# Performance work log

Hardware: AMD Instinct MI355X
Metric: run time of the kernel (lower is better)

The kernel has to match this reference:

```python
import jax, jax.numpy as jnp
import numpy as np
import math

D = 768
H = 12
DFF = 3072
HD = D // H


def _layernorm(x, g, b, eps=1e-5):
    mu = jnp.mean(x, axis=-1, keepdims=True)
    var = jnp.var(x, axis=-1, keepdims=True)
    return (x - mu) * jax.lax.rsqrt(var + eps) * g + b


def setup_inputs() -> dict:
    key = jax.random.key(0)
    ks = jax.random.split(key, 12)
    B, S = 2, 4096
    s = 1.0 / math.sqrt(D)
    sf = 1.0 / math.sqrt(DFF)
    return {
        "x": jax.random.normal(ks[0], (B, S, D), jnp.float32),
        "attention_mask": jnp.ones((B, S), jnp.int32),
        "ln1_g": jnp.ones((D,), jnp.float32),
        "ln1_b": jnp.zeros((D,), jnp.float32),
        "ln2_g": jnp.ones((D,), jnp.float32),
        "ln2_b": jnp.zeros((D,), jnp.float32),
        "Wq": jax.random.normal(ks[1], (D, D), jnp.float32) * s,
        "bq": jnp.zeros((D,), jnp.float32),
        "Wk": jax.random.normal(ks[2], (D, D), jnp.float32) * s,
        "bk": jnp.zeros((D,), jnp.float32),
        "Wv": jax.random.normal(ks[3], (D, D), jnp.float32) * s,
        "bv": jnp.zeros((D,), jnp.float32),
        "Wo": jax.random.normal(ks[4], (D, D), jnp.float32) * s,
        "bo": jnp.zeros((D,), jnp.float32),
        "W1": jax.random.normal(ks[5], (D, DFF), jnp.float32) * s,
        "b1": jnp.zeros((DFF,), jnp.float32),
        "W2": jax.random.normal(ks[6], (DFF, D), jnp.float32) * sf,
        "b2": jnp.zeros((D,), jnp.float32),
    }


def _block(x, attention_mask, ln1_g, ln1_b, ln2_g, ln2_b,
           Wq, bq, Wk, bk, Wv, bv, Wo, bo, W1, b1, W2, b2):
    B, S, _ = x.shape
    h = _layernorm(x, ln1_g, ln1_b)
    q = (h @ Wq + bq).reshape(B, S, H, HD)
    k = (h @ Wk + bk).reshape(B, S, H, HD)
    v = (h @ Wv + bv).reshape(B, S, H, HD)
    # scores: [B, H, S, S]
    dots = jnp.einsum('bqhd,bkhd->bhqk', q, k) / math.sqrt(HD)
    causal = jnp.tril(jnp.ones((S, S), bool))  # True = keep
    keep = causal[None, None] & (attention_mask != 0)[:, None, None, :]
    dots = jnp.where(keep, dots, -jnp.inf)
    probs = jax.nn.softmax(dots, axis=-1)
    ctx = jnp.einsum('bhqk,bkhd->bqhd', probs, v).reshape(B, S, D)
    sa = ctx @ Wo + bo  # dropout = identity (eval)
    x = x + sa
    h2 = _layernorm(x, ln2_g, ln2_b)
    ff = jax.nn.relu(h2 @ W1 + b1) @ W2 + b2
    return x + ff


def reference(x, attention_mask, ln1_g, ln1_b, ln2_g, ln2_b,
              Wq, bq, Wk, bk, Wv, bv, Wo, bo, W1, b1, W2, b2):
    return _block(x, attention_mask, ln1_g, ln1_b, ln2_g, ln2_b,
                  Wq, bq, Wk, bk, Wv, bv, Wo, bo, W1, b1, W2, b2)
```

## Files before the change

### kernel.cpp

```cpp
#include <hip/hip_runtime.h>
#include <hip/hip_bf16.h>
#include <math.h>

#define S_LEN 4096
#define DMODEL 768
#define NHEAD 12
#define HDIM 64
#define DFF_ 3072
#define MROWS 8192

typedef __bf16 bf16;
typedef __bf16 bf16x4 __attribute__((ext_vector_type(4)));
typedef __bf16 bf16x8 __attribute__((ext_vector_type(8)));
typedef float f32x4 __attribute__((ext_vector_type(4)));
typedef float f32x16 __attribute__((ext_vector_type(16)));
typedef short s16x4 __attribute__((ext_vector_type(4)));
typedef s16x4 frag4;

union F4 { float4 v; float f[4]; };
union U2 { bf16 h[2]; unsigned u; };
union P4 { unsigned u[2]; frag4 v; };

__device__ __forceinline__ void gld_lds16(void* lds, const void* g) {
    __builtin_amdgcn_global_load_lds(
        (const __attribute__((address_space(1))) unsigned int*)g,
        (__attribute__((address_space(3))) unsigned int*)lds, 16, 0, 0);
}

__device__ __forceinline__ f32x4 mfma16(frag4 a, frag4 b, f32x4 c) {
#if __has_builtin(__builtin_amdgcn_mfma_f32_16x16x16bf16_1k)
    return __builtin_amdgcn_mfma_f32_16x16x16bf16_1k(a, b, c, 0, 0, 0);
#else
    union { frag4 s; bf16x4 h; } ua, ub; ua.s = a; ub.s = b;
    bf16x8 a8 = {ua.h[0], ua.h[1], ua.h[2], ua.h[3],
                 (bf16)0.f, (bf16)0.f, (bf16)0.f, (bf16)0.f};
    bf16x8 b8 = {ub.h[0], ub.h[1], ub.h[2], ub.h[3],
                 (bf16)0.f, (bf16)0.f, (bf16)0.f, (bf16)0.f};
    return __builtin_amdgcn_mfma_f32_16x16x32_bf16(a8, b8, c, 0, 0, 0);
#endif
}

__global__ __launch_bounds__(256) void pre_kernel(
    const float* __restrict__ Wq, const float* __restrict__ Wk,
    const float* __restrict__ Wv, const float* __restrict__ Wo,
    const float* __restrict__ W1, const float* __restrict__ W2,
    bf16* __restrict__ Wqt, bf16* __restrict__ Wkt, bf16* __restrict__ Wvt,
    bf16* __restrict__ Wot, bf16* __restrict__ W1t, bf16* __restrict__ W2t,
    const float* __restrict__ x, const float* __restrict__ g,
    const float* __restrict__ bta, bf16* __restrict__ hout) {
    const int tid = threadIdx.x;
    if (blockIdx.x < 1728) {
        int t = blockIdx.x;
        const float* W; bf16* Wt; int K, N;
        if      (t < 144)  { W = Wq; Wt = Wqt; K = 768;  N = 768;  }
        else if (t < 288)  { W = Wk; Wt = Wkt; K = 768;  N = 768;  t -= 144; }
        else if (t < 432)  { W = Wv; Wt = Wvt; K = 768;  N = 768;  t -= 288; }
        else if (t < 576)  { W = Wo; Wt = Wot; K = 768;  N = 768;  t -= 432; }
        else if (t < 1152) { W = W1; Wt = W1t; K = 768;  N = 3072; t -= 576; }
        else               { W = W2; Wt = W2t; K = 3072; N = 768;  t -= 1152; }
        const int nx = N >> 6;
        const int n0 = (t % nx) * 64, k0 = (t / nx) * 64;
        __shared__ float tile[64][65];
        const int lr = tid >> 4, lc = (tid & 15) << 2;
#pragma unroll
        for (int i = 0; i < 4; ++i) {
            const int r = lr + i * 16;
            F4 w; w.v = *(const float4*)&W[(size_t)(k0 + r) * N + n0 + lc];
#pragma unroll
            for (int j = 0; j < 4; ++j) tile[r][lc + j] = w.f[j];
        }
        __syncthreads();
#pragma unroll
        for (int i = 0; i < 4; ++i) {
            const int n = lr + i * 16;
            bf16x4 o;
#pragma unroll
            for (int j = 0; j < 4; ++j) o[j] = (bf16)tile[lc + j][n];
            *(bf16x4*)&Wt[(size_t)(n0 + n) * K + k0 + lc] = o;
        }
    } else {
        const int row = blockIdx.x - 1728;
        const float* xr = x + (size_t)row * DMODEL;
        float v0 = xr[tid], v1 = xr[tid + 256], v2 = xr[tid + 512];
        float s = v0 + v1 + v2;
        float ss = v0 * v0 + v1 * v1 + v2 * v2;
        for (int o = 32; o > 0; o >>= 1) {
            s += __shfl_down(s, o, 64);
            ss += __shfl_down(ss, o, 64);
        }
        __shared__ float sm[4], sm2[4];
        const int w = tid >> 6, lane = tid & 63;
        if (lane == 0) { sm[w] = s; sm2[w] = ss; }
        __syncthreads();
        s = sm[0] + sm[1] + sm[2] + sm[3];
        ss = sm2[0] + sm2[1] + sm2[2] + sm2[3];
        const float mu = s * (1.0f / DMODEL);
        const float var = ss * (1.0f / DMODEL) - mu * mu;
        const float rs = rsqrtf(var + 1e-5f);
        bf16* orow = hout + (size_t)row * DMODEL;
        orow[tid]       = (bf16)((v0 - mu) * rs * g[tid]       + bta[tid]);
        orow[tid + 256] = (bf16)((v1 - mu) * rs * g[tid + 256] + bta[tid + 256]);
        orow[tid + 512] = (bf16)((v2 - mu) * rs * g[tid + 512] + bta[tid + 512]);
    }
}

template<typename OUT>
__global__ __launch_bounds__(256) void ln_kernel(const float* __restrict__ x,
                                                 const float* __restrict__ g,
                                                 const float* __restrict__ bta,
                                                 OUT* __restrict__ out,
                                                 float* __restrict__ zb) {
    const int row = blockIdx.x;
    const int t = threadIdx.x;
    const float* xr = x + (size_t)row * DMODEL;
    float v0 = xr[t], v1 = xr[t + 256], v2 = xr[t + 512];
    float s = v0 + v1 + v2;
    float ss = v0 * v0 + v1 * v1 + v2 * v2;
    for (int o = 32; o > 0; o >>= 1) {
        s += __shfl_down(s, o, 64);
        ss += __shfl_down(ss, o, 64);
    }
    __shared__ float sm[4], sm2[4];
    const int w = t >> 6, lane = t & 63;
    if (lane == 0) { sm[w] = s; sm2[w] = ss; }
    __syncthreads();
    s = sm[0] + sm[1] + sm[2] + sm[3];
    ss = sm2[0] + sm2[1] + sm2[2] + sm2[3];
    const float mu = s * (1.0f / DMODEL);
    const float var = ss * (1.0f / DMODEL) - mu * mu;
    const float rs = rsqrtf(var + 1e-5f);
    OUT* orow = out + (size_t)row * DMODEL;
    orow[t]       = (OUT)((v0 - mu) * rs * g[t]       + bta[t]);
    orow[t + 256] = (OUT)((v1 - mu) * rs * g[t + 256] + bta[t + 256]);
    orow[t + 512] = (OUT)((v2 - mu) * rs * g[t + 512] + bta[t + 512]);
}

__global__ __launch_bounds__(256) void vtrans_kernel(const bf16* __restrict__ vb,
                                                     bf16* __restrict__ vbt) {
    const int kt = blockIdx.x, h = blockIdx.y, b = blockIdx.z;
    __shared__ bf16 tile[64][65];
    const int t = threadIdx.x;
    const int kl = t >> 2, ds = (t & 3) * 16;
    const bf16* src = vb + (size_t)(b * S_LEN + kt * 64 + kl) * DMODEL + h * HDIM + ds;
    *(bf16x8*)&tile[kl][ds]     = *(const bf16x8*)src;
    *(bf16x8*)&tile[kl][ds + 8] = *(const bf16x8*)(src + 8);
    __syncthreads();
    const int d = t >> 2;
    bf16* drow = vbt + (size_t)((b * NHEAD + h) * HDIM + d) * S_LEN + kt * 64;
#pragma unroll
    for (int c = 0; c < 2; ++c) {
        const int k0 = (t & 3) * 16 + c * 8;
        bf16x8 o;
#pragma unroll
        for (int j = 0; j < 8; ++j) o[j] = tile[k0 + j][d];
        *(bf16x8*)(drow + k0) = o;
    }
}

template<int MT, bool RELU, bool RES, bool OUT_BF16>
__global__ __launch_bounds__(256) void mgemm_kernel(
    const bf16* __restrict__ A,
    const bf16* __restrict__ Wt0, const float* __restrict__ bias0, void* __restrict__ C0,
    const bf16* __restrict__ Wt1, const float* __restrict__ bias1, void* __restrict__ C1,
    const bf16* __restrict__ Wt2, const float* __restrict__ bias2, void* __restrict__ C2,
    const float* __restrict__ R, int M, int N, int K, int Kloop,
    int koff0, int koff1, int koff2,
    float sc0, float sc1, float sc2) {
    const bf16* Wt = Wt0; const float* bias = bias0; void* C = C0; float sc = sc0; int koff = koff0;
    if (blockIdx.z == 1) { Wt = Wt1; bias = bias1; C = C1; sc = sc1; koff = koff1; }
    if (blockIdx.z == 2) { Wt = Wt2; bias = bias2; C = C2; sc = sc2; koff = koff2; }

    const int gx = gridDim.x;
    const int nwg = gx * gridDim.y;
    const int chunk = nwg >> 3;
    int lid = blockIdx.y * gx + blockIdx.x;
    lid = (lid & 7) * chunk + (lid >> 3);
    const int row0 = (lid / gx) * MT, col0 = (lid % gx) * 128;

    constexpr int NI = (MT == 128) ? 2 : 1;
    __shared__ bf16 As[2][MT * 32];
    __shared__ bf16 Bs[2][128 * 32];

    const int tid = threadIdx.x;
    const int wave = tid >> 6, lane = tid & 63;
    const int wr = (MT == 128) ? (wave >> 1) * 64 : 0;
    const int wc = (MT == 128) ? (wave & 1) * 64 : wave * 32;
    const int r5 = lane & 31, khalf = lane >> 5;
    const int rsw = (r5 >> 1) & 3;

    const int st_row = (lane >> 2);
    const int st_off = (((lane & 3) ^ ((lane >> 3) & 3)) << 4);

    f32x16 acc[2][NI] = {};

    const char* Ab = (const char*)(A + (size_t)row0 * K + koff);
    const char* Bb = (const char*)(Wt + (size_t)col0 * K + koff);
    const size_t strideA = (size_t)K * 2;

    for (int k0 = 0; k0 < Kloop; k0 += 64) {
#pragma unroll
        for (int s = 0; s < 2; ++s) {
            const int kk = k0 + s * 32;
            if (MT == 128) {
#pragma unroll
                for (int issue = 0; issue < 2; ++issue) {
                    const int r = wave * 32 + issue * 16 + st_row;
                    gld_lds16((char*)As[s] + (wave * 32 + issue * 16) * 64,
                              Ab + (size_t)r * strideA + kk * 2 + st_off);
                }
            } else {
                const int r = wave * 16 + st_row;
                gld_lds16((char*)As[s] + (wave * 16) * 64,
                          Ab + (size_t)r * strideA + kk * 2 + st_off);
            }
#pragma unroll
            for (int issue = 0; issue < 2; ++issue) {
                const int r = wave * 32 + issue * 16 + st_row;
                gld_lds16((char*)Bs[s] + (wave * 32 + issue * 16) * 64,
                          Bb + (size_t)r * strideA + kk * 2 + st_off);
            }
        }
        __syncthreads();
#pragma unroll
        for (int s = 0; s < 2; ++s) {
            bf16x8 af[2][2], bfr[NI][2];
#pragma unroll
            for (int mi = 0; mi < 2; ++mi)
#pragma unroll
                for (int kc = 0; kc < 2; ++kc)
                    af[mi][kc] = *(const bf16x8*)((const char*)As[s] +
                        (wr + mi * 32 + r5) * 64 + (((kc * 2 + khalf) ^ rsw) << 4));
#pragma unroll
            for (int ni = 0; ni < NI; ++ni)
#pragma unroll
                for (int kc = 0; kc < 2; ++kc)
                    bfr[ni][kc] = *(const bf16x8*)((const char*)Bs[s] +
                        (wc + ni * 32 + r5) * 64 + (((kc * 2 + khalf) ^ rsw) << 4));
#pragma unroll
            for (int mi = 0; mi < 2; ++mi)
#pragma unroll
                for (int ni = 0; ni < NI; ++ni)
#pragma unroll
                    for (int kc = 0; kc < 2; ++kc)
                        acc[mi][ni] = __builtin_amdgcn_mfma_f32_32x32x16_bf16(
                            bfr[ni][kc], af[mi][kc], acc[mi][ni], 0, 0, 0);
        }
        __syncthreads();
    }

#pragma unroll
    for (int ni = 0; ni < NI; ++ni) {
#pragma unroll
        for (int g = 0; g < 4; ++g) {
            const int col = col0 + wc + ni * 32 + g * 8 + khalf * 4;
            F4 bv4; bv4.v = *(const float4*)&bias[col];
#pragma unroll
            for (int mi = 0; mi < 2; ++mi) {
                const int row = row0 + wr + mi * 32 + r5;
                F4 o;
#pragma unroll
                for (int r = 0; r < 4; ++r) o.f[r] = acc[mi][ni][g * 4 + r] + bv4.f[r];
                if (RES) {
                    F4 rr; rr.v = *(const float4*)&R[(size_t)row * N + col];
#pragma unroll
                    for (int r = 0; r < 4; ++r) o.f[r] += rr.f[r];
                }
#pragma unroll
                for (int r = 0; r < 4; ++r) {
                    o.f[r] *= sc;
                    if (RELU) o.f[r] = fmaxf(o.f[r], 0.0f);
                }
                if (OUT_BF16) {
                    bf16x4 ob;
#pragma unroll
                    for (int r = 0; r < 4; ++r) ob[r] = (bf16)o.f[r];
                    *(bf16x4*)&((bf16*)C)[(size_t)row * N + col] = ob;
                } else {
                    *(float4*)&((float*)C)[(size_t)row * N + col] = o.v;
                }
            }
        }
    }
}

__global__ __launch_bounds__(256) void mattn_kernel(
    const bf16* __restrict__ Q, const bf16* __restrict__ K,
    const bf16* __restrict__ Vt, const int* __restrict__ amask,
    bf16* __restrict__ O) {
    const int bx = blockIdx.x, h = blockIdx.y, b = blockIdx.z;

    __shared__ bf16 Ks[2][4096];
    __shared__ bf16 Vs[2][4096];
    __shared__ bf16 Os[64][68];
    __shared__ float mk[2][64];
    __shared__ int flagv[2];

    const int tid = threadIdx.x;
    const int wave = tid >> 6, lane = tid & 63;
    const int l = lane & 15, quad = lane >> 4;
    const float NEG_INF = -__builtin_huge_valf();

    const int g1 = 256 + tid;
    const int rw0 = tid >> 3, pc0 = tid & 7;
    const int rw1 = g1 >> 3,  pc1 = g1 & 7;
    const int koff0 = rw0 * DMODEL + ((pc0 ^ (rw0 & 7)) << 3);
    const int koff1 = rw1 * DMODEL + ((pc1 ^ (rw1 & 7)) << 3);
    const int voff0 = rw0 * S_LEN + ((pc0 ^ (rw0 & 7)) << 3);
    const int voff1 = rw1 * S_LEN + ((pc1 ^ (rw1 & 7)) << 3);

    const bf16* Kbase = K + (size_t)b * S_LEN * DMODEL + h * HDIM;
    const bf16* Vtb = Vt + (size_t)((b * NHEAD + h) * HDIM) * S_LEN;

    const int sw = (l & 7) << 4;
    const int krd0 = l * 128 + ((quad << 4) ^ sw);
    const int krd1 = l * 128 + (((4 + quad) << 4) ^ sw);

    P4 onesu; onesu.u[0] = 0x3F803F80u; onesu.u[1] = 0x3F803F80u;
    const frag4 onesA = onesu.v;

#pragma unroll 1
    for (int pass = 0; pass < 2; ++pass) {
        const int qt = pass ? bx : (63 - bx);

        const bf16* Qb = Q + (size_t)(b * S_LEN + qt * 64 + wave * 16 + l) * DMODEL + h * HDIM;
        const bf16x8 qf0 = *(const bf16x8*)(Qb + quad * 8);
        const bf16x8 qf1 = *(const bf16x8*)(Qb + 32 + quad * 8);

        float m_run = NEG_INF;
        f32x4 acc[4] = {};
        f32x4 acc_l = {};

        {
            char* kd = (char*)Ks[0] + wave * 1024;
            char* vd = (char*)Vs[0] + wave * 1024;
            gld_lds16(kd,        Kbase + koff0);
            gld_lds16(kd + 4096, Kbase + koff1);
            gld_lds16(vd,        Vtb + voff0);
            gld_lds16(vd + 4096, Vtb + voff1);
            if (wave == 0) {
                int mv0 = amask[b * S_LEN + lane];
                mk[0][lane] = mv0 ? 0.0f : NEG_INF;
                unsigned long long bal = __ballot(mv0 != 0);
                if (lane == 0) flagv[0] = (bal == ~0ULL);
            }
        }
        __syncthreads();
        int buf = 0;
        int mv = 1;

        for (int kt = 0; kt <= qt; ++kt) {
            const bool more = (kt < qt);
            if (more) {
                const bf16* kg = Kbase + (size_t)(kt + 1) * 64 * DMODEL;
                const bf16* vg = Vtb + (kt + 1) * 64;
                const int nb = buf ^ 1;
                char* kd = (char*)Ks[nb] + wave * 1024;
                char* vd = (char*)Vs[nb] + wave * 1024;
                gld_lds16(kd,        kg + koff0);
                gld_lds16(kd + 4096, kg + koff1);
                gld_lds16(vd,        vg + voff0);
                gld_lds16(vd + 4096, vg + voff1);
                if (wave == 0) mv = amask[b * S_LEN + (kt + 1) * 64 + lane];
            }

            const int allv = flagv[buf];
            const char* Ksb = (const char*)Ks[buf];
            const char* Vsb = (const char*)Vs[buf];
            f32x4 sreg[4] = {};
            __builtin_amdgcn_s_setprio(1);
#pragma unroll
            for (int mi = 0; mi < 4; ++mi) {
                bf16x8 kf0 = *(const bf16x8*)(Ksb + mi * 2048 + krd0);
                bf16x8 kf1 = *(const bf16x8*)(Ksb + mi * 2048 + krd1);
                sreg[mi] = __builtin_amdgcn_mfma_f32_16x16x32_bf16(kf0, qf0, sreg[mi], 0, 0, 0);
                sreg[mi] = __builtin_amdgcn_mfma_f32_16x16x32_bf16(kf1, qf1, sreg[mi], 0, 0, 0);
            }
            __builtin_amdgcn_s_setprio(0);
            if (!allv) {
#pragma unroll
                for (int mi = 0; mi < 4; ++mi) {
                    F4 m4; m4.v = *(const float4*)&mk[buf][mi * 16 + quad * 4];
#pragma unroll
                    for (int r = 0; r < 4; ++r) sreg[mi][r] += m4.f[r];
                }
            }
            if (kt == qt) {
#pragma unroll
                for (int mi = 0; mi < 4; ++mi)
#pragma unroll
                    for (int r = 0; r < 4; ++r)
                        if (mi * 16 + quad * 4 + r > wave * 16 + l)
                            sreg[mi][r] = NEG_INF;
            }

            float mloc = sreg[0][0];
#pragma unroll
            for (int mi = 0; mi < 4; ++mi)
#pragma unroll
                for (int r = 0; r < 4; ++r) mloc = fmaxf(mloc, sreg[mi][r]);
            mloc = fmaxf(mloc, __shfl_xor(mloc, 16, 64));
            mloc = fmaxf(mloc, __shfl_xor(mloc, 32, 64));
            if (__any(mloc > m_run + 8.0f)) {
                const float mn = fmaxf(m_run, mloc);
                const float alpha = __builtin_amdgcn_exp2f(m_run - mn);
                m_run = mn;
#pragma unroll
                for (int di = 0; di < 4; ++di)
#pragma unroll
                    for (int r = 0; r < 4; ++r) acc[di][r] *= alpha;
#pragma unroll
                for (int r = 0; r < 4; ++r) acc_l[r] *= alpha;
            }
#pragma unroll
            for (int mi = 0; mi < 4; ++mi)
#pragma unroll
                for (int r = 0; r < 4; ++r)
                    sreg[mi][r] = __builtin_amdgcn_exp2f(sreg[mi][r] - m_run);

            unsigned pk[4][2];
#pragma unroll
            for (int mi = 0; mi < 4; ++mi) {
                U2 w0; w0.h[0] = (bf16)sreg[mi][0]; w0.h[1] = (bf16)sreg[mi][1];
                U2 w1; w1.h[0] = (bf16)sreg[mi][2]; w1.h[1] = (bf16)sreg[mi][3];
                pk[mi][0] = w0.u; pk[mi][1] = w1.u;
            }

            __builtin_amdgcn_s_setprio(1);
#pragma unroll
            for (int mi = 0; mi < 4; ++mi) {
                P4 pb; pb.u[0] = pk[mi][0]; pb.u[1] = pk[mi][1];
                const int vb_mi = (((mi << 5) | (quad << 3)) ^ sw);
#pragma unroll
                for (int di = 0; di < 4; ++di) {
                    frag4 va = *(const frag4*)(Vsb + di * 2048 + l * 128 + vb_mi);
                    acc[di] = mfma16(va, pb.v, acc[di]);
                }
                acc_l = mfma16(onesA, pb.v, acc_l);
            }
            __builtin_amdgcn_s_setprio(0);

            if (more && wave == 0) {
                const int nb = buf ^ 1;
                mk[nb][lane] = mv ? 0.0f : NEG_INF;
                unsigned long long bal = __ballot(mv != 0);
                if (lane == 0) flagv[nb] = (bal == ~0ULL);
            }
            __syncthreads();
            buf ^= 1;
        }

        const float l_fin = __shfl(acc_l[0], l, 64);
        const float rinv = 1.0f / l_fin;
#pragma unroll
        for (int mi = 0; mi < 4; ++mi) {
            U2 w0; w0.h[0] = (bf16)(acc[mi][0] * rinv); w0.h[1] = (bf16)(acc[mi][1] * rinv);
            U2 w1; w1.h[0] = (bf16)(acc[mi][2] * rinv); w1.h[1] = (bf16)(acc[mi][3] * rinv);
            *(unsigned*)&Os[wave * 16 + l][mi * 16 + quad * 4]     = w0.u;
            *(unsigned*)&Os[wave * 16 + l][mi * 16 + quad * 4 + 2] = w1.u;
        }
        __syncthreads();
        {
            const int orow = tid >> 2, oseg = (tid & 3) * 16;
            bf16* Og = O + (size_t)(b * S_LEN + qt * 64 + orow) * DMODEL + h * HDIM + oseg;
            *(bf16x8*)Og       = *(const bf16x8*)&Os[orow][oseg];
            *(bf16x8*)(Og + 8) = *(const bf16x8*)&Os[orow][oseg + 8];
        }
        __syncthreads();
    }
}

extern "C" void kernel_launch(void* const* d_in, const int* in_sizes, int n_in,
                              void* d_out, int out_size, void* d_ws, size_t ws_size,
                              hipStream_t stream) {
    const float* x     = (const float*)d_in[0];
    const int*   amask = (const int*)  d_in[1];
    const float* ln1_g = (const float*)d_in[2];
    const float* ln1_b = (const float*)d_in[3];
    const float* ln2_g = (const float*)d_in[4];
    const float* ln2_b = (const float*)d_in[5];
    const float* Wq = (const float*)d_in[6];  const float* bq = (const float*)d_in[7];
    const float* Wk = (const float*)d_in[8];  const float* bk = (const float*)d_in[9];
    const float* Wv = (const float*)d_in[10]; const float* bv = (const float*)d_in[11];
    const float* Wo = (const float*)d_in[12]; const float* bo = (const float*)d_in[13];
    const float* W1 = (const float*)d_in[14]; const float* b1 = (const float*)d_in[15];
    const float* W2 = (const float*)d_in[16]; const float* b2 = (const float*)d_in[17];
    float* out = (float*)d_out;

    char* ws = (char*)d_ws;
    const size_t WSML = (size_t)DMODEL * DMODEL * 2;
    const size_t WBIG = (size_t)DMODEL * DFF_ * 2;
    bf16* Wqt = (bf16*)(ws + 0 * WSML);
    bf16* Wkt = (bf16*)(ws + 1 * WSML);
    bf16* Wvt = (bf16*)(ws + 2 * WSML);
    bf16* Wot = (bf16*)(ws + 3 * WSML);
    bf16* W1t = (bf16*)(ws + 4 * WSML);
    bf16* W2t = (bf16*)(ws + 4 * WSML + WBIG);
    char* act = ws + 4 * WSML + 2 * WBIG;

    const size_t HB = (size_t)MROWS * DMODEL * 2;
    const size_t FB = (size_t)MROWS * DMODEL * 4;
    bf16*  h    = (bf16*)(act);
    bf16*  qb   = (bf16*)(act + HB);
    bf16*  kb   = (bf16*)(act + 2 * HB);
    bf16*  vb   = (bf16*)(act + 3 * HB);
    bf16*  ctx  = h;
    float* x1   = (float*)(act + 4 * HB);
    bf16*  f    = (bf16*)(act + 4 * HB + FB);
    bf16*  h2   = h;
    bf16*  vbt  = f;

    const float SCL = 0.125f * 1.44269504089f;

    pre_kernel<<<1728 + MROWS, 256, 0, stream>>>(Wq, Wk, Wv, Wo, W1, W2,
                                                 Wqt, Wkt, Wvt, Wot, W1t, W2t,
                                                 x, ln1_g, ln1_b, h);
    mgemm_kernel<128, false, false, true><<<dim3(DMODEL / 128, MROWS / 128, 3), 256, 0, stream>>>(
        h, Wqt, bq, qb, Wkt, bk, kb, Wvt, bv, vb, nullptr,
        MROWS, DMODEL, DMODEL, DMODEL, 0, 0, 0, SCL, 1.0f, 1.0f);
    vtrans_kernel<<<dim3(S_LEN / 64, NHEAD, 2), 256, 0, stream>>>(vb, vbt);
    mattn_kernel<<<dim3(32, NHEAD, 2), 256, 0, stream>>>(qb, kb, vbt, amask, ctx);
    mgemm_kernel<64, false, true, false><<<dim3(DMODEL / 128, MROWS / 64, 1), 256, 0, stream>>>(
        ctx, Wot, bo, x1, Wot, bo, x1, Wot, bo, x1, x,
        MROWS, DMODEL, DMODEL, DMODEL, 0, 0, 0, 1.0f, 1.0f, 1.0f);
    ln_kernel<bf16><<<MROWS, 256, 0, stream>>>(x1, ln2_g, ln2_b, h2, nullptr);
    mgemm_kernel<128, true, false, true><<<dim3(DFF_ / 128, MROWS / 128, 1), 256, 0, stream>>>(
        h2, W1t, b1, f, W1t, b1, f, W1t, b1, f, nullptr,
        MROWS, DFF_, DMODEL, DMODEL, 0, 0, 0, 1.0f, 1.0f, 1.0f);
    mgemm_kernel<64, false, true, false><<<dim3(DMODEL / 128, MROWS / 64, 1), 256, 0, stream>>>(
        f, W2t, b2, out, W2t, b2, out, W2t, b2, out, x1,
        MROWS, DMODEL, DFF_, DFF_, 0, 0, 0, 1.0f, 1.0f, 1.0f);
}
```

Before: 469.4 us.

## Fuse V transpose into QKV GEMM epilogue and switch GEMMs to 16x16x32 MFMA

Removes the separate V transpose kernel. The QKV GEMM now writes V directly in head-major transposed layout, with operands swapped in the MFMA for the V slice. All GEMMs move from 32x32x16 MFMA tiles to 16x16x32 tiles with a new fragment layout, and the LDS XOR swizzle on staging is dropped. This saves a launch and a round trip of V through memory, but unswizzled LDS reads may cause bank conflicts and the transposed stores are strided.

Result: faster. 451.9 us (-3.7%).

```diff
diff --git a/kernel.cpp b/kernel.cpp
--- a/kernel.cpp
+++ b/kernel.cpp
@@ -13,7 +13,6 @@
 typedef __bf16 bf16x4 __attribute__((ext_vector_type(4)));
 typedef __bf16 bf16x8 __attribute__((ext_vector_type(8)));
 typedef float f32x4 __attribute__((ext_vector_type(4)));
-typedef float f32x16 __attribute__((ext_vector_type(16)));
 typedef short s16x4 __attribute__((ext_vector_type(4)));
 typedef s16x4 frag4;
 
@@ -135,29 +134,7 @@
     orow[t + 512] = (OUT)((v2 - mu) * rs * g[t + 512] + bta[t + 512]);
 }
 
-__global__ __launch_bounds__(256) void vtrans_kernel(const bf16* __restrict__ vb,
-                                                     bf16* __restrict__ vbt) {
-    const int kt = blockIdx.x, h = blockIdx.y, b = blockIdx.z;
-    __shared__ bf16 tile[64][65];
-    const int t = threadIdx.x;
-    const int kl = t >> 2, ds = (t & 3) * 16;
-    const bf16* src = vb + (size_t)(b * S_LEN + kt * 64 + kl) * DMODEL + h * HDIM + ds;
-    *(bf16x8*)&tile[kl][ds]     = *(const bf16x8*)src;
-    *(bf16x8*)&tile[kl][ds + 8] = *(const bf16x8*)(src + 8);
-    __syncthreads();
-    const int d = t >> 2;
-    bf16* drow = vbt + (size_t)((b * NHEAD + h) * HDIM + d) * S_LEN + kt * 64;
-#pragma unroll
-    for (int c = 0; c < 2; ++c) {
-        const int k0 = (t & 3) * 16 + c * 8;
-        bf16x8 o;
-#pragma unroll
-        for (int j = 0; j < 8; ++j) o[j] = tile[k0 + j][d];
-        *(bf16x8*)(drow + k0) = o;
-    }
-}
-
-template<int MT, bool RELU, bool RES, bool OUT_BF16>
+template<int MT, bool RELU, bool RES, bool OUT_BF16, bool VT>
 __global__ __launch_bounds__(256) void mgemm_kernel(
     const bf16* __restrict__ A,
     const bf16* __restrict__ Wt0, const float* __restrict__ bias0, void* __restrict__ C0,
@@ -169,6 +146,7 @@
     const bf16* Wt = Wt0; const float* bias = bias0; void* C = C0; float sc = sc0; int koff = koff0;
     if (blockIdx.z == 1) { Wt = Wt1; bias = bias1; C = C1; sc = sc1; koff = koff1; }
     if (blockIdx.z == 2) { Wt = Wt2; bias = bias2; C = C2; sc = sc2; koff = koff2; }
+    const bool vt = VT && (blockIdx.z == 2);
 
     const int gx = gridDim.x;
     const int nwg = gx * gridDim.y;
@@ -177,7 +155,7 @@
     lid = (lid & 7) * chunk + (lid >> 3);
     const int row0 = (lid / gx) * MT, col0 = (lid % gx) * 128;
 
-    constexpr int NI = (MT == 128) ? 2 : 1;
+    constexpr int NI = (MT == 128) ? 4 : 2;
     __shared__ bf16 As[2][MT * 32];
     __shared__ bf16 Bs[2][128 * 32];
 
@@ -185,13 +163,12 @@
     const int wave = tid >> 6, lane = tid & 63;
     const int wr = (MT == 128) ? (wave >> 1) * 64 : 0;
     const int wc = (MT == 128) ? (wave & 1) * 64 : wave * 32;
-    const int r5 = lane & 31, khalf = lane >> 5;
-    const int rsw = (r5 >> 1) & 3;
+    const int mrow = lane & 15, kq = (lane >> 4) * 8;
 
     const int st_row = (lane >> 2);
-    const int st_off = (((lane & 3) ^ ((lane >> 3) & 3)) << 4);
-
-    f32x16 acc[2][NI] = {};
+    const int st_off = (lane & 3) * 16;
+
+    f32x4 acc[4][NI] = {};
 
     const char* Ab = (const char*)(A + (size_t)row0 * K + koff);
     const char* Bb = (const char*)(Wt + (size_t)col0 * K + koff);
@@ -223,61 +200,78 @@
         __syncthreads();
 #pragma unroll
         for (int s = 0; s < 2; ++s) {
-            bf16x8 af[2][2], bfr[NI][2];
-#pragma unroll
-            for (int mi = 0; mi < 2; ++mi)
-#pragma unroll
-                for (int kc = 0; kc < 2; ++kc)
-                    af[mi][kc] = *(const bf16x8*)((const char*)As[s] +
-                        (wr + mi * 32 + r5) * 64 + (((kc * 2 + khalf) ^ rsw) << 4));
+            bf16x8 af[4], bfr[NI];
+#pragma unroll
+            for (int mi = 0; mi < 4; ++mi)
+                af[mi] = *(const bf16x8*)&As[s][(wr + mi * 16 + mrow) * 32 + kq];
 #pragma unroll
             for (int ni = 0; ni < NI; ++ni)
-#pragma unroll
-                for (int kc = 0; kc < 2; ++kc)
-                    bfr[ni][kc] = *(const bf16x8*)((const char*)Bs[s] +
-                        (wc + ni * 32 + r5) * 64 + (((kc * 2 + khalf) ^ rsw) << 4));
-#pragma unroll
-            for (int mi = 0; mi < 2; ++mi)
-#pragma unroll
-                for (int ni = 0; ni < NI; ++ni)
-#pragma unroll
-                    for (int kc = 0; kc < 2; ++kc)
-                        acc[mi][ni] = __builtin_amdgcn_mfma_f32_32x32x16_bf16(
-                            bfr[ni][kc], af[mi][kc], acc[mi][ni], 0, 0, 0);
+                bfr[ni] = *(const bf16x8*)&Bs[s][(wc + ni * 16 + mrow) * 32 + kq];
+            if (vt) {
+#pragma unroll
+                for (int mi = 0; mi < 4; ++mi)
+#pragma unroll
+                    for (int ni = 0; ni < NI; ++ni)
+                        acc[mi][ni] = __builtin_amdgcn_mfma_f32_16x16x32_bf16(
+                            af[mi], bfr[ni], acc[mi][ni], 0, 0, 0);
+            } else {
+#pragma unroll
+                for (int mi = 0; mi < 4; ++mi)
+#pragma unroll
+                    for (int ni = 0; ni < NI; ++ni)
+                        acc[mi][ni] = __builtin_amdgcn_mfma_f32_16x16x32_bf16(
+                            bfr[ni], af[mi], acc[mi][ni], 0, 0, 0);
+            }
         }
         __syncthreads();
     }
 
+    const int quad = lane >> 4;
+    if (vt) {
+#pragma unroll
+        for (int ni = 0; ni < NI; ++ni) {
+            const int c = col0 + wc + ni * 16 + mrow;
+            const float bvv = bias[c];
+            const int hh = c >> 6, dl = c & 63;
+#pragma unroll
+            for (int mi = 0; mi < 4; ++mi) {
+                const int tok = row0 + wr + mi * 16 + quad * 4;
+                const int bb = tok >> 12, ss = tok & 4095;
+                bf16x4 ob;
+#pragma unroll
+                for (int r = 0; r < 4; ++r) ob[r] = (bf16)(acc[mi][ni][r] + bvv);
+                *(bf16x4*)&((bf16*)C)[(size_t)((bb * NHEAD + hh) * HDIM + dl) * S_LEN + ss] = ob;
+            }
+        }
+        return;
+    }
 #pragma unroll
     for (int ni = 0; ni < NI; ++ni) {
-#pragma unroll
-        for (int g = 0; g < 4; ++g) {
-            const int col = col0 + wc + ni * 32 + g * 8 + khalf * 4;
-            F4 bv4; bv4.v = *(const float4*)&bias[col];
-#pragma unroll
-            for (int mi = 0; mi < 2; ++mi) {
-                const int row = row0 + wr + mi * 32 + r5;
-                F4 o;
-#pragma unroll
-                for (int r = 0; r < 4; ++r) o.f[r] = acc[mi][ni][g * 4 + r] + bv4.f[r];
-                if (RES) {
-                    F4 rr; rr.v = *(const float4*)&R[(size_t)row * N + col];
-#pragma unroll
-                    for (int r = 0; r < 4; ++r) o.f[r] += rr.f[r];
-                }
-#pragma unroll
-                for (int r = 0; r < 4; ++r) {
-                    o.f[r] *= sc;
-                    if (RELU) o.f[r] = fmaxf(o.f[r], 0.0f);
-                }
-                if (OUT_BF16) {
-                    bf16x4 ob;
-#pragma unroll
-                    for (int r = 0; r < 4; ++r) ob[r] = (bf16)o.f[r];
-                    *(bf16x4*)&((bf16*)C)[(size_t)row * N + col] = ob;
-                } else {
-                    *(float4*)&((float*)C)[(size_t)row * N + col] = o.v;
-                }
+        const int col = col0 + wc + ni * 16 + quad * 4;
+        F4 bv4; bv4.v = *(const float4*)&bias[col];
+#pragma unroll
+        for (int mi = 0; mi < 4; ++mi) {
+            const int row = row0 + wr + mi * 16 + mrow;
+            F4 o;
+#pragma unroll
+            for (int r = 0; r < 4; ++r) o.f[r] = acc[mi][ni][r] + bv4.f[r];
+            if (RES) {
+                F4 rr; rr.v = *(const float4*)&R[(size_t)row * N + col];
+#pragma unroll
+                for (int r = 0; r < 4; ++r) o.f[r] += rr.f[r];
+            }
+#pragma unroll
+            for (int r = 0; r < 4; ++r) {
+                o.f[r] *= sc;
+                if (RELU) o.f[r] = fmaxf(o.f[r], 0.0f);
+            }
+            if (OUT_BF16) {
+                bf16x4 ob;
+#pragma unroll
+                for (int r = 0; r < 4; ++r) ob[r] = (bf16)o.f[r];
+                *(bf16x4*)&((bf16*)C)[(size_t)row * N + col] = ob;
+            } else {
+                *(float4*)&((float*)C)[(size_t)row * N + col] = o.v;
             }
         }
     }
@@ -508,25 +502,25 @@
     bf16*  f    = (bf16*)(act + 4 * HB + FB);
     bf16*  h2   = h;
     bf16*  vbt  = f;
+    (void)vb;
 
     const float SCL = 0.125f * 1.44269504089f;
 
     pre_kernel<<<1728 + MROWS, 256, 0, stream>>>(Wq, Wk, Wv, Wo, W1, W2,
                                                  Wqt, Wkt, Wvt, Wot, W1t, W2t,
                                                  x, ln1_g, ln1_b, h);
-    mgemm_kernel<128, false, false, true><<<dim3(DMODEL / 128, MROWS / 128, 3), 256, 0, stream>>>(
-        h, Wqt, bq, qb, Wkt, bk, kb, Wvt, bv, vb, nullptr,
+    mgemm_kernel<128, false, false, true, true><<<dim3(DMODEL / 128, MROWS / 128, 3), 256, 0, stream>>>(
+        h, Wqt, bq, qb, Wkt, bk, kb, Wvt, bv, vbt, nullptr,
         MROWS, DMODEL, DMODEL, DMODEL, 0, 0, 0, SCL, 1.0f, 1.0f);
-    vtrans_kernel<<<dim3(S_LEN / 64, NHEAD, 2), 256, 0, stream>>>(vb, vbt);
     mattn_kernel<<<dim3(32, NHEAD, 2), 256, 0, stream>>>(qb, kb, vbt, amask, ctx);
-    mgemm_kernel<64, false, true, false><<<dim3(DMODEL / 128, MROWS / 64, 1), 256, 0, stream>>>(
+    mgemm_kernel<64, false, true, false, false><<<dim3(DMODEL / 128, MROWS / 64, 1), 256, 0, stream>>>(
         ctx, Wot, bo, x1, Wot, bo, x1, Wot, bo, x1, x,
         MROWS, DMODEL, DMODEL, DMODEL, 0, 0, 0, 1.0f, 1.0f, 1.0f);
     ln_kernel<bf16><<<MROWS, 256, 0, stream>>>(x1, ln2_g, ln2_b, h2, nullptr);
-    mgemm_kernel<128, true, false, true><<<dim3(DFF_ / 128, MROWS / 128, 1), 256, 0, stream>>>(
+    mgemm_kernel<128, true, false, true, false><<<dim3(DFF_ / 128, MROWS / 128, 1), 256, 0, stream>>>(
         h2, W1t, b1, f, W1t, b1, f, W1t, b1, f, nullptr,
         MROWS, DFF_, DMODEL, DMODEL, 0, 0, 0, 1.0f, 1.0f, 1.0f);
-    mgemm_kernel<64, false, true, false><<<dim3(DMODEL / 128, MROWS / 64, 1), 256, 0, stream>>>(
+    mgemm_kernel<64, false, true, false, false><<<dim3(DMODEL / 128, MROWS / 64, 1), 256, 0, stream>>>(
         f, W2t, b2, out, W2t, b2, out, W2t, b2, out, x1,
         MROWS, DMODEL, DFF_, DFF_, 0, 0, 0, 1.0f, 1.0f, 1.0f);
 }
```
